# Kernel optimization log

Measured on AMD Instinct MI355X. Metric: run time of the kernel, lower is better.

Reference implementation:

```python
import jax, jax.numpy as jnp
import numpy as np

KERNEL = 3          # route_nms_kernel
MAX_ROUTES = 256    # max_routes (topk per image)
STRIDE = 4.0        # route_stride
MIN_SIZE = 32.0     # route_min_size
MAX_SIZE = 512.0    # route_max_size
POWER = 2.0         # route_score_power
B, H, W = 32, 512, 512


def setup_inputs() -> dict:
    key = jax.random.key(0)
    k1, k2, k3 = jax.random.split(key, 3)
    return {
        "route_logits": jax.random.normal(k1, (B, 1, H, W), dtype=jnp.float32),
        "scale_logits": jax.random.normal(k2, (B, 1, H, W), dtype=jnp.float32),
        "uncertainty_logits": jax.random.normal(k3, (B, 1, H, W), dtype=jnp.float32),
        "image_h": 2048,
        "image_w": 2048,
    }


def _local_max_pool(x):
    # x: [H, W]; 3x3 max pool, stride 1, pad kernel//2 (torch F.max_pool2d pads with -inf)
    pad = KERNEL // 2
    return jax.lax.reduce_window(x, -jnp.inf, jax.lax.max,
                                 (KERNEL, KERNEL), (1, 1),
                                 [(pad, pad), (pad, pad)])


def reference(route_logits, scale_logits, uncertainty_logits, image_h, image_w):
    # score_map = sigmoid(logits)^power * (1 - 0.35*sigmoid(uncertainty))  (use_route_uncertainty=True)
    score_map = jnp.power(jax.nn.sigmoid(route_logits), POWER)
    score_map = score_map * (1.0 - 0.35 * jax.nn.sigmoid(uncertainty_logits))
    img_h = jnp.float32(image_h)
    img_w = jnp.float32(image_w)
    width = route_logits.shape[-1]

    def per_image(batch_idx, scores2d, scale2d, unc2d):
        pooled = _local_max_pool(scores2d)
        filtered = jnp.where(scores2d == pooled, scores2d, -1.0)  # masked_fill(~mask, -1)
        values, indices = jax.lax.top_k(filtered.reshape(-1), MAX_ROUTES)
        valid = values > 0.0  # torch filters values>0; here kept as fixed-shape mask
        ys = indices // width
        xs = indices % width
        cx = (xs.astype(jnp.float32) + 0.5) * STRIDE
        cy = (ys.astype(jnp.float32) + 0.5) * STRIDE
        scale_g = scale2d[ys, xs]
        unc = jax.nn.sigmoid(unc2d[ys, xs])
        side = MIN_SIZE + jax.nn.sigmoid(scale_g) * (MAX_SIZE - MIN_SIZE)
        side = side * (1.0 + 0.25 * unc)
        half = side * 0.5
        x1 = jnp.clip(cx - half, 0.0, img_w - 1.0)
        y1 = jnp.clip(cy - half, 0.0, img_h - 1.0)
        x2 = jnp.clip(cx + half, 1.0, img_w)
        y2 = jnp.clip(cy + half, 1.0, img_h)
        rois = jnp.stack([jnp.full_like(x1, batch_idx), x1, y1, x2, y2], axis=1)  # [K,5]
        rois = jnp.where(valid[:, None], rois, 0.0)
        vals = jnp.where(valid, values, 0.0)
        return rois, vals, valid

    batch_ids = jnp.arange(route_logits.shape[0], dtype=jnp.float32)
    rois, scores, valid = jax.vmap(per_image)(
        batch_ids, score_map[:, 0], scale_logits[:, 0], uncertainty_logits[:, 0])
    # rois: [B, K, 5], scores: [B, K], valid: [B, K] (per_image_counts = valid.sum(-1))
    return rois, scores, valid
```

## Files before the change

kernel.cpp:

```cpp
#include <hip/hip_runtime.h>
#include <cstdint>
#include <cstddef>

#define BATCH 32
#define IMH 512
#define IMW 512
#define KMAX 256

#define TILE_ROWS 16
#define NBLKX 2
#define NYB (IMH / TILE_ROWS)
#define NL1 (NBLKX * NYB * 4)
#define NM1 (NL1 / 4)
#define NMID (NM1 / 4)
#define WCAP 256
#define SSTRIDE 260

#define TPB2 512

typedef unsigned long long u64;

__device__ __forceinline__ float sigmoidf_(float x) {
    return 1.0f / (1.0f + expf(-x));
}
__device__ __forceinline__ float scoref_(float r, float u) {
    const float sg = sigmoidf_(r);
    return sg * sg * (1.0f - 0.35f * sigmoidf_(u));
}

#define SHF(v, jj, dm) do {                                         \
    const u64 o_ = __shfl_xor((v), (jj), 64);                       \
    const bool take_ = ((((lane & (jj)) == 0) == (dm)) == ((v) < o_)); \
    (v) = take_ ? o_ : (v);                                         \
} while (0)

#define RMAX(a, b) do {                                             \
    const u64 hi_ = ((a) > (b)) ? (a) : (b);                        \
    const u64 lo_ = ((a) > (b)) ? (b) : (a);                        \
    (a) = hi_; (b) = lo_;                                           \
} while (0)

#define RMIN(a, b) do {                                             \
    const u64 hi_ = ((a) > (b)) ? (a) : (b);                        \
    const u64 lo_ = ((a) > (b)) ? (b) : (a);                        \
    (a) = lo_; (b) = hi_;                                           \
} while (0)

__device__ __forceinline__ void clean256(u64& v0, u64& v1, u64& v2, u64& v3,
                                         const int lane) {
    RMAX(v0, v2); RMAX(v1, v3);
    RMAX(v0, v1); RMAX(v2, v3);
    #pragma unroll
    for (int j = 32; j > 0; j >>= 1) {
        SHF(v0, j, true); SHF(v1, j, true); SHF(v2, j, true); SHF(v3, j, true);
    }
}

__device__ __forceinline__ void sort256(u64& v0, u64& v1, u64& v2, u64& v3,
                                        const int lane) {
    #pragma unroll
    for (int k = 2; k <= 32; k <<= 1) {
        #pragma unroll
        for (int j = k >> 1; j > 0; j >>= 1) {
            const bool dm = ((lane & k) == 0);
            SHF(v0, j, dm); SHF(v1, j, dm); SHF(v2, j, dm); SHF(v3, j, dm);
        }
    }
    #pragma unroll
    for (int j = 32; j > 0; j >>= 1) {
        SHF(v0, j, true); SHF(v1, j, false); SHF(v2, j, true); SHF(v3, j, false);
    }
    RMAX(v0, v1); RMIN(v2, v3);
    #pragma unroll
    for (int j = 32; j > 0; j >>= 1) {
        SHF(v0, j, true); SHF(v1, j, true); SHF(v2, j, false); SHF(v3, j, false);
    }
    clean256(v0, v1, v2, v3, lane);
}

__device__ __forceinline__ void sort128(u64& v0, u64& v1, const int lane) {
    #pragma unroll
    for (int k = 2; k <= 32; k <<= 1) {
        #pragma unroll
        for (int j = k >> 1; j > 0; j >>= 1) {
            const bool dm = ((lane & k) == 0);
            SHF(v0, j, dm); SHF(v1, j, dm);
        }
    }
    #pragma unroll
    for (int j = 32; j > 0; j >>= 1) {
        SHF(v0, j, true); SHF(v1, j, false);
    }
    RMAX(v0, v1);
    #pragma unroll
    for (int j = 32; j > 0; j >>= 1) {
        SHF(v0, j, true); SHF(v1, j, true);
    }
}

__device__ __forceinline__ void merge256(u64& v0, u64& v1, u64& v2, u64& v3,
                                         u64 w0, u64 w1, u64 w2, u64 w3,
                                         const int lane) {
    const int rl = 63 ^ lane;
    const u64 b0 = __shfl(w3, rl, 64);
    const u64 b1 = __shfl(w2, rl, 64);
    const u64 b2 = __shfl(w1, rl, 64);
    const u64 b3 = __shfl(w0, rl, 64);
    v0 = (v0 > b0) ? v0 : b0;
    v1 = (v1 > b1) ? v1 : b1;
    v2 = (v2 > b2) ? v2 : b2;
    v3 = (v3 > b3) ? v3 : b3;
    clean256(v0, v1, v2, v3, lane);
}

__device__ __forceinline__ void load256(const u64* p, u64& v0, u64& v1,
                                        u64& v2, u64& v3, const int lane) {
    v0 = p[lane]; v1 = p[lane + 64]; v2 = p[lane + 128]; v3 = p[lane + 192];
}
__device__ __forceinline__ void store256(u64* p, u64 v0, u64 v1,
                                         u64 v2, u64 v3, const int lane) {
    p[lane] = v0; p[lane + 64] = v1; p[lane + 128] = v2; p[lane + 192] = v3;
}

__device__ __forceinline__ void merge4s(const u64* p,
                                        u64& a0, u64& a1, u64& a2, u64& a3,
                                        const int lane) {
    load256(p, a0, a1, a2, a3, lane);
    u64 w0, w1, w2, w3;
    load256(p + KMAX, w0, w1, w2, w3, lane);
    merge256(a0, a1, a2, a3, w0, w1, w2, w3, lane);
    u64 c0, c1, c2, c3;
    load256(p + 2 * KMAX, c0, c1, c2, c3, lane);
    load256(p + 3 * KMAX, w0, w1, w2, w3, lane);
    merge256(c0, c1, c2, c3, w0, w1, w2, w3, lane);
    merge256(a0, a1, a2, a3, c0, c1, c2, c3, lane);
}

__global__ __launch_bounds__(256)
void score_nms_kernel(const float* __restrict__ route,
                      const float* __restrict__ unc,
                      u64* __restrict__ top) {
    const int b    = blockIdx.z;
    const int t    = threadIdx.x;
    const int w    = t >> 6;
    const int lane = t & 63;
    const int X0   = blockIdx.x * 256;
    const int Y0   = blockIdx.y * TILE_ROWS;

    __shared__ float sT[18][SSTRIDE];
    __shared__ float eL[18], eR[18];
    __shared__ u64 lcand[4 * WCAP];
    u64* myR = lcand + w * WCAP;

    const float* rB = route + (size_t)b * IMH * IMW;
    const float* uB = unc   + (size_t)b * IMH * IMW;

    #pragma unroll
    for (int k = 0; k < 5; ++k) {
        const int r = 4 * k + w;
        if (r < 18) {
            const int y = Y0 - 1 + r;
            float4 s4 = make_float4(-INFINITY, -INFINITY, -INFINITY, -INFINITY);
            if (y >= 0 && y < IMH) {
                const size_t o = (size_t)y * IMW + X0 + 4 * lane;
                const float4 r4 = *(const float4*)(rB + o);
                const float4 u4 = *(const float4*)(uB + o);
                s4.x = scoref_(r4.x, u4.x);
                s4.y = scoref_(r4.y, u4.y);
                s4.z = scoref_(r4.z, u4.z);
                s4.w = scoref_(r4.w, u4.w);
            }
            *(float4*)&sT[r][4 * lane] = s4;
        }
    }
    if (t < 36) {
        const int p = t >> 1, side = t & 1;
        const int y = Y0 - 1 + p;
        const int x = side ? (X0 + 256) : (X0 - 1);
        float s = -INFINITY;
        if (y >= 0 && y < IMH && x >= 0 && x < IMW)
            s = scoref_(rB[(size_t)y * IMW + x], uB[(size_t)y * IMW + x]);
        if (side) eR[p] = s; else eL[p] = s;
    }
    __syncthreads();

    const u64 laneMaskLt = (1ull << lane) - 1ull;
    int wcnt = 0;

    float hmP[4], hmC[4], hmN[4], sC[4], sN[4];

    #define LOADROW2(rr, hm, sq) do {                                       \
        const float4 q_ = *(const float4*)&sT[(rr)][4 * lane];              \
        float lft_ = __shfl_up(q_.w, 1, 64);                                \
        if (lane == 0) lft_ = eL[(rr)];                                     \
        float rgt_ = __shfl_down(q_.x, 1, 64);                              \
        if (lane == 63) rgt_ = eR[(rr)];                                    \
        (hm)[0] = fmaxf(fmaxf(lft_, q_.x), q_.y);                           \
        (hm)[1] = fmaxf(fmaxf(q_.x, q_.y), q_.z);                           \
        (hm)[2] = fmaxf(fmaxf(q_.y, q_.z), q_.w);                           \
        (hm)[3] = fmaxf(fmaxf(q_.z, q_.w), rgt_);                           \
        (sq)[0] = q_.x; (sq)[1] = q_.y; (sq)[2] = q_.z; (sq)[3] = q_.w;     \
    } while (0)

    {
        float dump[4];
        LOADROW2(4 * w,     hmP, dump);
        LOADROW2(4 * w + 1, hmC, sC);
    }
    #pragma unroll
    for (int i = 0; i < 4; ++i) {
        LOADROW2(4 * w + 2 + i, hmN, sN);

        const int yo = Y0 + 4 * w + i;
        bool p[4]; int cntT = 0;
        #pragma unroll
        for (int j = 0; j < 4; ++j) {
            const float m9 = fmaxf(fmaxf(hmP[j], hmC[j]), hmN[j]);
            p[j] = (sC[j] >= m9);
            cntT += p[j] ? 1 : 0;
        }
        const u64 B0 = __ballot(cntT & 1);
        const u64 B1 = __ballot(cntT & 2);
        const u64 B2 = __ballot(cntT & 4);
        const int total = __popcll(B0) + 2 * __popcll(B1) + 4 * __popcll(B2);
        if (total > 0) {
            const int prefix = __popcll(B0 & laneMaskLt) + 2 * __popcll(B1 & laneMaskLt)
                             + 4 * __popcll(B2 & laneMaskLt);
            int mb = wcnt + prefix;
            #pragma unroll
            for (int j = 0; j < 4; ++j) {
                if (p[j]) {
                    const unsigned idx = (unsigned)(yo * IMW + (X0 + 4 * lane + j));
                    const u64 key = ((u64)__float_as_uint(sC[j]) << 32) | (unsigned)(~idx);
                    if (mb < WCAP) myR[mb] = key;
                    ++mb;
                }
            }
            wcnt += total;
        }

        #pragma unroll
        for (int j = 0; j < 4; ++j) { hmP[j] = hmC[j]; hmC[j] = hmN[j]; sC[j] = sN[j]; }
    }
    #undef LOADROW2

    const int m = (wcnt < WCAP) ? wcnt : WCAP;
    u64 a0, a1, a2, a3;
    if (m <= 128) {
        a0 = (lane      < m) ? myR[lane]      : 0ull;
        a1 = (lane + 64 < m) ? myR[lane + 64] : 0ull;
        sort128(a0, a1, lane);
        a2 = 0ull; a3 = 0ull;
    } else {
        a0 = (lane       < m) ? myR[lane]       : 0ull;
        a1 = (lane + 64  < m) ? myR[lane + 64]  : 0ull;
        a2 = (lane + 128 < m) ? myR[lane + 128] : 0ull;
        a3 = (lane + 192 < m) ? myR[lane + 192] : 0ull;
        sort256(a0, a1, a2, a3, lane);
    }

    const int list = (blockIdx.y * 4 + w) * NBLKX + blockIdx.x;
    u64* seg = top + ((size_t)b * NL1 + list) * KMAX;
    store256(seg, a0, a1, a2, a3, lane);
}

__global__ __launch_bounds__(128)
void merge4_kernel(const u64* __restrict__ in, int nin,
                   u64* __restrict__ out_) {
    const int w    = threadIdx.x >> 6;
    const int lane = threadIdx.x & 63;
    const int o    = blockIdx.x * 2 + w;
    const int b    = blockIdx.y;
    const int nout = nin / 4;
    if (o >= nout) return;

    const u64* L = in + ((size_t)b * nin + o * 4) * KMAX;
    u64 a0, a1, a2, a3;
    merge4s(L, a0, a1, a2, a3, lane);

    u64* out = out_ + ((size_t)b * nout + o) * KMAX;
    store256(out, a0, a1, a2, a3, lane);
}

__global__ __launch_bounds__(TPB2)
void tail_kernel(const u64* __restrict__ mid,
                 const float* __restrict__ scale,
                 const float* __restrict__ unc,
                 const int* __restrict__ imh,
                 const int* __restrict__ imw,
                 float* __restrict__ rois,
                 float* __restrict__ scoresOut,
                 float* __restrict__ validOut) {
    const int b   = blockIdx.x;
    const int tid = threadIdx.x;

    __shared__ u64 bufA[NMID * KMAX];
    __shared__ u64 bufB[(NMID / 2) * KMAX];

    const u64* tb = mid + (size_t)b * NMID * KMAX;
    for (int i = tid; i < NMID * KMAX; i += TPB2) bufA[i] = tb[i];
    __syncthreads();

    u64* src = bufA;
    u64* dst = bufB;
    int nl = NMID;
    while (nl > 1) {
        const int half = nl >> 1;
        const int E = half * KMAX;
        for (int p = tid; p < E; p += TPB2) {
            const int h = p >> 8;
            const int i = p & (KMAX - 1);
            const u64 a = src[(2 * h) * KMAX + i];
            const u64 c = src[(2 * h + 1) * KMAX + (KMAX - 1 - i)];
            dst[p] = (a > c) ? a : c;
        }
        __syncthreads();
        for (int j = KMAX >> 1; j > 0; j >>= 1) {
            for (int p = tid; p < (E >> 1); p += TPB2) {
                const int i   = ((p & ~(j - 1)) << 1) | (p & (j - 1));
                const int ixj = i | j;
                const u64 a = dst[i];
                const u64 c = dst[ixj];
                if (a < c) { dst[i] = c; dst[ixj] = a; }
            }
            __syncthreads();
        }
        u64* t = src; src = dst; dst = t;
        nl = half;
    }

    if (tid < KMAX) {
        const u64 k = src[tid];
        const float value = __uint_as_float((unsigned)(k >> 32));
        const bool valid  = (k != 0ull) && (value > 0.0f);

        float r0 = 0.f, r1 = 0.f, r2 = 0.f, r3 = 0.f, r4 = 0.f, sv = 0.f, vv = 0.f;
        if (valid) {
            const unsigned idx = ~(unsigned)(k & 0xFFFFFFFFull);
            const int y = (int)(idx / IMW);
            const int x = (int)(idx % IMW);
            const float cx = ((float)x + 0.5f) * 4.0f;
            const float cy = ((float)y + 0.5f) * 4.0f;
            const float sg = scale[(size_t)b * IMH * IMW + idx];
            const float uu = unc[(size_t)b * IMH * IMW + idx];
            const float su = sigmoidf_(uu);
            float side = 32.0f + sigmoidf_(sg) * (512.0f - 32.0f);
            side = side * (1.0f + 0.25f * su);
            const float half2 = side * 0.5f;
            const float fw = (float)imw[0];
            const float fh = (float)imh[0];
            r0 = (float)b;
            r1 = fminf(fmaxf(cx - half2, 0.0f), fw - 1.0f);
            r2 = fminf(fmaxf(cy - half2, 0.0f), fh - 1.0f);
            r3 = fminf(fmaxf(cx + half2, 1.0f), fw);
            r4 = fminf(fmaxf(cy + half2, 1.0f), fh);
            sv = value;
            vv = 1.0f;
        }
        float* roiP = rois + ((size_t)b * KMAX + tid) * 5;
        roiP[0] = r0; roiP[1] = r1; roiP[2] = r2; roiP[3] = r3; roiP[4] = r4;
        scoresOut[b * KMAX + tid] = sv;
        validOut[b * KMAX + tid]  = vv;
    }
}

extern "C" void kernel_launch(void* const* d_in, const int* in_sizes, int n_in,
                              void* d_out, int out_size, void* d_ws, size_t ws_size,
                              hipStream_t stream) {
    const float* route = (const float*)d_in[0];
    const float* scale = (const float*)d_in[1];
    const float* unc   = (const float*)d_in[2];
    const int*   imh   = (const int*)d_in[3];
    const int*   imw   = (const int*)d_in[4];

    u64* top  = (u64*)d_ws;
    u64* mid1 = top  + (size_t)BATCH * NL1 * KMAX;
    u64* mid2 = mid1 + (size_t)BATCH * NM1 * KMAX;

    float* rois      = (float*)d_out;
    float* scoresOut = rois + (size_t)BATCH * KMAX * 5;
    float* validOut  = scoresOut + (size_t)BATCH * KMAX;

    dim3 grid1(NBLKX, NYB, BATCH);
    score_nms_kernel<<<grid1, 256, 0, stream>>>(route, unc, top);

    dim3 grid2(NM1 / 2, BATCH);
    merge4_kernel<<<grid2, 128, 0, stream>>>(top, NL1, mid1);

    dim3 grid3(NMID / 2, BATCH);
    merge4_kernel<<<grid3, 128, 0, stream>>>(mid1, NM1, mid2);

    tail_kernel<<<BATCH, TPB2, 0, stream>>>(mid2, scale, unc,
                                            imh, imw, rois, scoresOut, validOut);
}
```

Baseline: 54.56 us.

## Merge the four per-wave top-k lists inside the score kernel

Each block of the scoring/NMS kernel now merges its four wave-local sorted candidate lists in shared memory through a two-level pairwise merge, and writes one list per block instead of four. This cuts global workspace traffic and removes one merge4 kernel launch from the reduction chain. The cost is extra __syncthreads barriers, and only some waves work during the in-block merge, which lengthens the first kernel.

```diff
diff --git a/kernel.cpp b/kernel.cpp
--- a/kernel.cpp
+++ b/kernel.cpp
@@ -10,9 +10,8 @@
 #define TILE_ROWS 16
 #define NBLKX 2
 #define NYB (IMH / TILE_ROWS)
-#define NL1 (NBLKX * NYB * 4)
-#define NM1 (NL1 / 4)
-#define NMID (NM1 / 4)
+#define NL1 (NBLKX * NYB)
+#define NMID (NL1 / 4)
 #define WCAP 256
 #define SSTRIDE 260
 
@@ -259,9 +258,27 @@
         sort256(a0, a1, a2, a3, lane);
     }
 
-    const int list = (blockIdx.y * 4 + w) * NBLKX + blockIdx.x;
-    u64* seg = top + ((size_t)b * NL1 + list) * KMAX;
-    store256(seg, a0, a1, a2, a3, lane);
+    __syncthreads();
+    store256(myR, a0, a1, a2, a3, lane);
+    __syncthreads();
+
+    if ((w & 1) == 0) {
+        u64 w0r, w1r, w2r, w3r;
+        load256(lcand + (w + 1) * WCAP, w0r, w1r, w2r, w3r, lane);
+        merge256(a0, a1, a2, a3, w0r, w1r, w2r, w3r, lane);
+        if (w == 2) store256(lcand + 2 * WCAP, a0, a1, a2, a3, lane);
+    }
+    __syncthreads();
+
+    if (w == 0) {
+        u64 w0r, w1r, w2r, w3r;
+        load256(lcand + 2 * WCAP, w0r, w1r, w2r, w3r, lane);
+        merge256(a0, a1, a2, a3, w0r, w1r, w2r, w3r, lane);
+
+        const int list = blockIdx.y * NBLKX + blockIdx.x;
+        u64* seg = top + ((size_t)b * NL1 + list) * KMAX;
+        store256(seg, a0, a1, a2, a3, lane);
+    }
 }
 
 __global__ __launch_bounds__(128)
@@ -373,9 +390,8 @@
     const int*   imh   = (const int*)d_in[3];
     const int*   imw   = (const int*)d_in[4];
 
-    u64* top  = (u64*)d_ws;
-    u64* mid1 = top  + (size_t)BATCH * NL1 * KMAX;
-    u64* mid2 = mid1 + (size_t)BATCH * NM1 * KMAX;
+    u64* top = (u64*)d_ws;
+    u64* mid = top + (size_t)BATCH * NL1 * KMAX;
 
     float* rois      = (float*)d_out;
     float* scoresOut = rois + (size_t)BATCH * KMAX * 5;
@@ -384,12 +400,9 @@
     dim3 grid1(NBLKX, NYB, BATCH);
     score_nms_kernel<<<grid1, 256, 0, stream>>>(route, unc, top);
 
-    dim3 grid2(NM1 / 2, BATCH);
-    merge4_kernel<<<grid2, 128, 0, stream>>>(top, NL1, mid1);
-
-    dim3 grid3(NMID / 2, BATCH);
-    merge4_kernel<<<grid3, 128, 0, stream>>>(mid1, NM1, mid2);
-
-    tail_kernel<<<BATCH, TPB2, 0, stream>>>(mid2, scale, unc,
+    dim3 grid2(NMID / 2, BATCH);
+    merge4_kernel<<<grid2, 128, 0, stream>>>(top, NL1, mid);
+
+    tail_kernel<<<BATCH, TPB2, 0, stream>>>(mid, scale, unc,
                                             imh, imw, rois, scoresOut, validOut);
 }
```

After: 52.37 us. 1.04x faster.
